# Optimization experiments

Hardware: AMD Instinct MI355X
Metric: run time of the kernel (lower is better)

Reference implementation:

```python
import jax, jax.numpy as jnp
import numpy as np

EPS = 1e-5

def conv(x, w, stride=1, pad=0, groups=1):
    # x: NCHW, w: OIHW
    return jax.lax.conv_general_dilated(
        x, w, window_strides=(stride, stride),
        padding=[(pad, pad), (pad, pad)],
        dimension_numbers=("NCHW", "OIHW", "NCHW"),
        feature_group_count=groups)

def bn_eval(x, gamma, beta, mean, var):
    scale = (gamma / jnp.sqrt(var + EPS))[None, :, None, None]
    shift = (beta - mean * gamma / jnp.sqrt(var + EPS))[None, :, None, None]
    return x * scale + shift

def setup_inputs() -> dict:
    key = jax.random.key(0)
    ks = jax.random.split(key, 12)
    B, Cin, H, W = 32, 64, 56, 56
    hidden, red, Cout, K = 384, 16, 64, 3
    f32 = jnp.float32
    x = jax.random.normal(ks[0], (B, Cin, H, W), dtype=f32)
    w_exp = jax.random.normal(ks[1], (hidden, Cin, 3, 3), dtype=f32) * 0.05
    w_dw  = jax.random.normal(ks[2], (hidden, 1, K, K), dtype=f32) * 0.1
    w_se1 = jax.random.normal(ks[3], (red, hidden, 1, 1), dtype=f32) * 0.05
    w_se2 = jax.random.normal(ks[4], (hidden, red, 1, 1), dtype=f32) * 0.1
    w_pw  = jax.random.normal(ks[5], (Cout, hidden, 1, 1), dtype=f32) * 0.05
    def bn_params(k, c):
        k1, k2 = jax.random.split(k)
        return (jnp.ones((c,), f32), jnp.zeros((c,), f32),
                jax.random.normal(k1, (c,), dtype=f32) * 0.01,
                jax.random.uniform(k2, (c,), dtype=f32, minval=0.5, maxval=1.5))
    g1, b1, m1, v1 = bn_params(ks[6], hidden)
    g2, b2, m2, v2 = bn_params(ks[7], hidden)
    g3, b3, m3, v3 = bn_params(ks[8], Cout)
    return dict(x=x, w_exp=w_exp, g1=g1, b1=b1, m1=m1, v1=v1,
                w_dw=w_dw, g2=g2, b2=b2, m2=m2, v2=v2,
                w_se1=w_se1, w_se2=w_se2, w_pw=w_pw,
                g3=g3, b3=b3, m3=m3, v3=v3)

def reference(x, w_exp, g1, b1, m1, v1, w_dw, g2, b2, m2, v2,
              w_se1, w_se2, w_pw, g3, b3, m3, v3):
    hidden = w_exp.shape[0]
    # expand conv (3x3) + BN + SiLU
    h = jax.nn.silu(bn_eval(conv(x, w_exp, stride=1, pad=1), g1, b1, m1, v1))
    # depthwise conv + BN + SiLU
    d = jax.nn.silu(bn_eval(conv(h, w_dw, stride=1, pad=1, groups=hidden), g2, b2, m2, v2))
    # squeeze-excitation: global avg pool -> 1x1 -> SiLU -> 1x1 -> sigmoid -> scale
    s = jnp.mean(d, axis=(2, 3), keepdims=True)            # [B, hidden, 1, 1]
    s = jax.nn.silu(conv(s, w_se1))
    s = jax.nn.sigmoid(conv(s, w_se2))
    d = d * s
    # pointwise projection + BN
    y = bn_eval(conv(d, w_pw), g3, b3, m3, v3)
    # eval mode: stochastic_depth is identity; quant_skip == (identity-quantized) input
    return y + x
```

## Files before the change

### kernel.cpp

```cpp
#include <hip/hip_runtime.h>

typedef unsigned short u16;
typedef unsigned int u32;
typedef __attribute__((ext_vector_type(2))) u32 u32x2;
typedef __attribute__((ext_vector_type(4))) u32 u32x4;
typedef __attribute__((ext_vector_type(2))) float f32x2;
typedef __attribute__((ext_vector_type(4))) float f32x4;
typedef __attribute__((ext_vector_type(8))) short s16x8;

#define DEV __device__ __forceinline__

DEV float bflo(u32 u){ union{u32 i; float f;} c; c.i = u << 16; return c.f; }
DEV float bfhi(u32 u){ union{u32 i; float f;} c; c.i = u & 0xffff0000u; return c.f; }
DEV u16 f2b(float f){
  union{float f; u32 u;} c; c.f = f;
  u32 u = c.u;
  u32 r = (u + 0x7fffu + ((u >> 16) & 1u)) >> 16;
  return (u16)r;
}
DEV float fsilu(float v){ return v / (1.f + __expf(-v)); }

typedef const __attribute__((address_space(1))) u32 gu32;
typedef __attribute__((address_space(3))) u32 lu32;
DEV void gload16(const u32* g, u32* l) {
  __builtin_amdgcn_global_load_lds((gu32*)g, (lu32*)l, 16, 0, 0);
}

constexpr int Bn = 32, Cin = 64, H = 56, Wd = 56, HID = 384, CO = 64;
constexpr int HW = H * Wd;
constexpr float EPS = 1e-5f;

constexpr int XROW = 72 * 64;
constexpr int WTAP = 128 * 64;
constexpr int WOCT = 9 * WTAP;
constexpr int XTROW = 72 * 64;

__global__ __launch_bounds__(256) void k_prep_wbn(
    const float* __restrict__ w,
    const float* __restrict__ g1, const float* __restrict__ b1,
    const float* __restrict__ m1, const float* __restrict__ v1,
    const float* __restrict__ g3, const float* __restrict__ b3,
    const float* __restrict__ m3, const float* __restrict__ v3,
    u16* __restrict__ wt,
    float* __restrict__ sc1, float* __restrict__ sh1,
    float* __restrict__ sc3, float* __restrict__ sh3)
{
  const int blk = blockIdx.x;
  if (blk < 864) {
    int t = blk * 256 + threadIdx.x;
    int octile = t / WOCT, r = t - octile * WOCT;
    int tap = r / WTAP, r2 = r - tap * WTAP;
    int ocl = r2 >> 6, col = r2 & 63;
    int physo = col >> 3, j = col & 7;
    int olog = physo ^ (ocl & 7);
    int ic = olog * 8 + j;
    int oc = octile * 128 + ocl;
    wt[t] = f2b(w[(oc * Cin + ic) * 9 + tap]);
  } else {
    for (int t = threadIdx.x; t < HID; t += 256) {
      float sc = g1[t] * rsqrtf(v1[t] + EPS);
      sc1[t] = sc;
      sh1[t] = b1[t] - m1[t] * sc;
    }
    if (threadIdx.x < CO) {
      int t = threadIdx.x;
      float sc = g3[t] * rsqrtf(v3[t] + EPS);
      sc3[t] = sc;
      sh3[t] = b3[t] - m3[t] * sc;
    }
  }
}

__global__ __launch_bounds__(256) void k_prep_x(
    const float* __restrict__ x, u16* __restrict__ xt, int b0)
{
  const int row = blockIdx.x;
  const int b = blockIdx.y, gb = b0 + b;
  const int tid = threadIdx.x;
  u16* dst = xt + ((size_t)b * 58 + row) * XTROW;
  if (row == 0 || row == 57) {
    for (int i = tid; i < 2304; i += 256) ((u32*)dst)[i] = 0;
    return;
  }
  const int y = row - 1;
  __shared__ u16 sx[64 * 58];
  {
    const int ic = tid >> 2, seg = tid & 3;
    const float* xp = x + ((size_t)(gb * Cin + ic) * H + y) * Wd + seg * 14;
    #pragma unroll
    for (int t = 0; t < 14; ++t) sx[ic * 58 + seg * 14 + t] = f2b(xp[t]);
  }
  __syncthreads();
  #pragma unroll
  for (int it = 0; it < 18; ++it) {
    const int slot = it * 4 + (tid >> 6);
    const int j = tid & 63;
    u16 v = 0;
    if (slot >= 1 && slot <= 56) {
      int ic = (((j >> 3) ^ (slot & 7)) << 3) | (j & 7);
      v = sx[ic * 58 + (slot - 1)];
    }
    dst[slot * 64 + j] = v;
  }
}

__global__ __launch_bounds__(256, 2) void k_expand_mfma(
    const u16* __restrict__ xt, const u16* __restrict__ wt,
    const float* __restrict__ sc1, const float* __restrict__ sh1,
    u16* __restrict__ h, int b0)
{
  (void)b0;
  __shared__ u16 sB[4 * XROW];
  __shared__ u16 sA[2][WTAP];
  const int tid = threadIdx.x;
  const int ypair = blockIdx.x, b = blockIdx.y;
  const int y0 = ypair * 2;
  const int wave = tid >> 6, ln = tid & 63;
  const int wm = wave >> 1, wn = wave & 1;
  const int lane15 = ln & 15, quad = ln >> 4;

  {
    const u32* xsrc = (const u32*)(xt + ((size_t)b * 58 + y0) * XTROW);
    #pragma unroll
    for (int it = 0; it < 9; ++it) {
      int chunk = it * 256 + tid;
      gload16(xsrc + chunk * 4, (u32*)sB + (chunk & ~63) * 4);
    }
    const u32* wsrc = (const u32*)wt;
    #pragma unroll
    for (int it = 0; it < 4; ++it) {
      int chunk = it * 256 + tid;
      gload16(wsrc + chunk * 4, (u32*)sA[0] + (chunk & ~63) * 4);
    }
  }
  __syncthreads();

  const int y = y0 + wn;

  for (int octile = 0; octile < 3; ++octile) {
    f32x4 acc[4][4];
    #pragma unroll
    for (int ms = 0; ms < 4; ++ms)
      #pragma unroll
      for (int ns = 0; ns < 4; ++ns) acc[ms][ns] = (f32x4){0.f, 0.f, 0.f, 0.f};

    #pragma unroll
    for (int tap = 0; tap < 9; ++tap) {
      const int step = octile * 9 + tap;
      const int buf = (octile + tap) & 1;

      u32x4 pf0, pf1, pf2, pf3;
      const bool pre = (step < 26);
      if (pre) {
        const u16* wnx = wt + (size_t)(step + 1) * WTAP;
        pf0 = *(const u32x4*)&wnx[(0 * 256 + tid) * 8];
        pf1 = *(const u32x4*)&wnx[(1 * 256 + tid) * 8];
        pf2 = *(const u32x4*)&wnx[(2 * 256 + tid) * 8];
        pf3 = *(const u32x4*)&wnx[(3 * 256 + tid) * 8];
      }

      constexpr int dyv[9] = {0,0,0,1,1,1,2,2,2};
      constexpr int dxv[9] = {0,1,2,0,1,2,0,1,2};
      const int dy = dyv[tap], dx = dxv[tap];
      const u16* sAc = sA[buf];
      __builtin_amdgcn_s_setprio(1);
      #pragma unroll
      for (int kk = 0; kk < 2; ++kk) {
        s16x8 af[4], bf[4];
        #pragma unroll
        for (int ms = 0; ms < 4; ++ms) {
          int ocl = wm * 64 + ms * 16 + lane15;
          int po = (kk * 4 + quad) ^ (ocl & 7);
          af[ms] = *(const s16x8*)&sAc[ocl * 64 + po * 8];
        }
        #pragma unroll
        for (int ns = 0; ns < 4; ++ns) {
          int row = wn + dy;
          int slot = ns * 16 + lane15 + dx;
          int po = (kk * 4 + quad) ^ (slot & 7);
          bf[ns] = *(const s16x8*)&sB[(row * 72 + slot) * 64 + po * 8];
        }
        #pragma unroll
        for (int ms = 0; ms < 4; ++ms)
          #pragma unroll
          for (int ns = 0; ns < 4; ++ns)
            acc[ms][ns] = __builtin_amdgcn_mfma_f32_16x16x32_bf16(
                af[ms], bf[ns], acc[ms][ns], 0, 0, 0);
      }
      __builtin_amdgcn_s_setprio(0);

      if (pre) {
        u16* sAn = sA[buf ^ 1];
        *(u32x4*)&sAn[(0 * 256 + tid) * 8] = pf0;
        *(u32x4*)&sAn[(1 * 256 + tid) * 8] = pf1;
        *(u32x4*)&sAn[(2 * 256 + tid) * 8] = pf2;
        *(u32x4*)&sAn[(3 * 256 + tid) * 8] = pf3;
      }
      __syncthreads();
    }

    #pragma unroll
    for (int ms = 0; ms < 4; ++ms) {
      int oc0 = octile * 128 + wm * 64 + ms * 16 + quad * 4;
      f32x4 sc = *(const f32x4*)&sc1[oc0];
      f32x4 sh = *(const f32x4*)&sh1[oc0];
      float scr[4] = {sc.x, sc.y, sc.z, sc.w};
      float shr[4] = {sh.x, sh.y, sh.z, sh.w};
      #pragma unroll
      for (int ns = 0; ns < 4; ++ns) {
        int xg = ns * 16 + lane15;
        if (xg < Wd) {
          float av[4] = {acc[ms][ns].x, acc[ms][ns].y, acc[ms][ns].z, acc[ms][ns].w};
          #pragma unroll
          for (int r = 0; r < 4; ++r) {
            float val = fsilu(av[r] * scr[r] + shr[r]);
            h[((size_t)(b * HID + oc0 + r) * H + y) * Wd + xg] = f2b(val);
          }
        }
      }
    }
  }
}

__global__ __launch_bounds__(256) void k_dw(
    const u16* __restrict__ h, const float* __restrict__ wdw,
    const float* __restrict__ g2, const float* __restrict__ b2,
    const float* __restrict__ m2, const float* __restrict__ v2,
    u16* __restrict__ d, float* __restrict__ mean)
{
  __shared__ float red[4];
  const int tid = threadIdx.x;
  const int c = blockIdx.x, b = blockIdx.y;
  const u32* hp32 = (const u32*)(h + (size_t)(b * HID + c) * HW);

  f32x2 wv2[9];
  #pragma unroll
  for (int t = 0; t < 9; ++t) {
    float w = wdw[c * 9 + t];
    wv2[t] = (f32x2){w, w};
  }
  const float sc = g2[c] * rsqrtf(v2[c] + EPS);
  const float sh = b2[c] - m2[c] * sc;
  const f32x2 scv = (f32x2){sc, sc}, shv = (f32x2){sh, sh};

  float lsum = 0.f;
  if (tid < 224) {
    const int r7 = tid / 28;
    const int wd = tid - r7 * 28;
    const int r0 = r7 * 7;
    u32* dp32 = (u32*)(d + (size_t)(b * HID + c) * HW);

    auto loadrow = [&](int rr, f32x2* P) {
      u32 m = 0, c0 = 0, p = 0;
      if (rr >= 0 && rr < 56) {
        const u32* rp = hp32 + rr * 28;
        c0 = rp[wd];
        if (wd > 0)  m = rp[wd - 1];
        if (wd < 27) p = rp[wd + 1];
      }
      float f_hm = bfhi(m), f_lc = bflo(c0), f_hc = bfhi(c0), f_lp = bflo(p);
      P[0] = (f32x2){f_hm, f_lc};
      P[1] = (f32x2){f_lc, f_hc};
      P[2] = (f32x2){f_hc, f_lp};
    };

    f32x2 Pa[3], Pb[3], Pc[3];
    loadrow(r0 - 1, Pa);
    loadrow(r0,     Pb);
    f32x2 ls2 = (f32x2){0.f, 0.f};
    #pragma unroll
    for (int i = 0; i < 7; ++i) {
      loadrow(r0 + i + 1, Pc);
      f32x2 s = (f32x2){0.f, 0.f};
      #pragma unroll
      for (int dx = 0; dx < 3; ++dx) s = __builtin_elementwise_fma(Pa[dx], wv2[dx], s);
      #pragma unroll
      for (int dx = 0; dx < 3; ++dx) s = __builtin_elementwise_fma(Pb[dx], wv2[3 + dx], s);
      #pragma unroll
      for (int dx = 0; dx < 3; ++dx) s = __builtin_elementwise_fma(Pc[dx], wv2[6 + dx], s);
      f32x2 t = __builtin_elementwise_fma(s, scv, shv);
      f32x2 val;
      val.x = fsilu(t.x);
      val.y = fsilu(t.y);
      ls2 += val;
      u32 pk;
      asm("v_cvt_pk_bf16_f32 %0, %1, %2" : "=v"(pk) : "v"(val.x), "v"(val.y));
      dp32[(r0 + i) * 28 + wd] = pk;
      #pragma unroll
      for (int q = 0; q < 3; ++q) { Pa[q] = Pb[q]; Pb[q] = Pc[q]; }
    }
    lsum = ls2.x + ls2.y;
  }

  #pragma unroll
  for (int off = 32; off > 0; off >>= 1) lsum += __shfl_down(lsum, off);
  if ((tid & 63) == 0) red[tid >> 6] = lsum;
  __syncthreads();
  if (tid == 0)
    mean[b * HID + c] = (red[0] + red[1] + red[2] + red[3]) * (1.f / 3136.f);
}

constexpr int PWP = 392;

__global__ __launch_bounds__(256, 2) void k_pw_mfma(
    const u16* __restrict__ d, const float* __restrict__ mean,
    const float* __restrict__ w1, const float* __restrict__ w2,
    const float* __restrict__ wpw,
    const float* __restrict__ sc3, const float* __restrict__ sh3,
    const float* __restrict__ x, float* __restrict__ out, int b0)
{
  __shared__ u16 sAw[64 * PWP];
  __shared__ u32 dtw[4 * 1024];
  __shared__ float smn[HID];
  __shared__ float sps[16 * 17];
  __shared__ float ss1[16];
  __shared__ float ssf[HID];
  const int tid = threadIdx.x;
  const int b = blockIdx.y, gb = b0 + b;
  const int p0 = blockIdx.x * 256;
  const int wave = tid >> 6, ln = tid & 63;
  const int lane15 = ln & 15, quad = ln >> 4;

  for (int c = tid; c < HID; c += 256) smn[c] = mean[b * HID + c];
  __syncthreads();
  {
    int r = tid >> 4, j = tid & 15;
    float p = 0.f;
    for (int c = j; c < HID; c += 16) p += smn[c] * w1[r * HID + c];
    sps[r * 17 + j] = p;
  }
  __syncthreads();
  if (tid < 16) {
    float s = 0.f;
    #pragma unroll
    for (int q = 0; q < 16; ++q) s += sps[tid * 17 + q];
    ss1[tid] = fsilu(s);
  }
  __syncthreads();
  for (int c = tid; c < HID; c += 256) {
    float s = 0.f;
    #pragma unroll
    for (int q = 0; q < 16; ++q) s += ss1[q] * w2[c * 16 + q];
    ssf[c] = 1.f / (1.f + __expf(-s));
  }
  __syncthreads();

  {
    for (int i = tid; i < 6144; i += 256) {
      int e = i * 4, co = e / 384, k = e - co * 384;
      f32x4 wv = *(const f32x4*)&wpw[e];
      f32x4 sf = *(const f32x4*)&ssf[k];
      float s3 = sc3[co];
      u32x2 pk;
      pk.x = (u32)f2b(wv.x * sf.x * s3) | ((u32)f2b(wv.y * sf.y * s3) << 16);
      pk.y = (u32)f2b(wv.z * sf.z * s3) | ((u32)f2b(wv.w * sf.w * s3) << 16);
      *(u32x2*)&sAw[co * PWP + k] = pk;
    }
  }
  __syncthreads();

  f32x4 acc[4][4];
  #pragma unroll
  for (int ms = 0; ms < 4; ++ms)
    #pragma unroll
    for (int ns = 0; ns < 4; ++ns) acc[ms][ns] = (f32x4){0.f, 0.f, 0.f, 0.f};

  const int cpair8 = ln >> 3;
  const int pxo = (ln & 7) * 8;
  const int swz = ln & 3;
  const int pbase = p0 + wave * 64;
  u32* mydt = &dtw[wave * 1024];
  const bool ld_ok = (pbase + pxo + 8 <= HW);
  const u16* dbase = d + (size_t)b * HID * HW + pbase + pxo;

  u32x4 pr0[2], pr1[2];
  #pragma unroll
  for (int ci = 0; ci < 2; ++ci) {
    pr0[ci] = (u32x4){0,0,0,0}; pr1[ci] = (u32x4){0,0,0,0};
    if (ld_ok) {
      int c = 2 * (ci * 8 + cpair8);
      const u16* dpp = dbase + (size_t)c * HW;
      pr0[ci] = *(const u32x4*)dpp;
      pr1[ci] = *(const u32x4*)(dpp + HW);
    }
  }

  for (int ks = 0; ks < 12; ++ks) {
    #pragma unroll
    for (int ci = 0; ci < 2; ++ci) {
      int k4 = ci * 2 + (cpair8 >> 2);
      u32* w0 = &mydt[pxo * 16 + ((k4 ^ swz) << 2) + (cpair8 & 3)];
      u32x4 r0 = pr0[ci], r1 = pr1[ci];
      w0[0 * 16] = (r0.x & 0xffffu) | (r1.x << 16);
      w0[1 * 16] = (r0.x >> 16)     | (r1.x & 0xffff0000u);
      w0[2 * 16] = (r0.y & 0xffffu) | (r1.y << 16);
      w0[3 * 16] = (r0.y >> 16)     | (r1.y & 0xffff0000u);
      w0[4 * 16] = (r0.z & 0xffffu) | (r1.z << 16);
      w0[5 * 16] = (r0.z >> 16)     | (r1.z & 0xffff0000u);
      w0[6 * 16] = (r0.w & 0xffffu) | (r1.w << 16);
      w0[7 * 16] = (r0.w >> 16)     | (r1.w & 0xffff0000u);
    }
    if (ks < 11) {
      #pragma unroll
      for (int ci = 0; ci < 2; ++ci) {
        if (ld_ok) {
          int c = (ks + 1) * 32 + 2 * (ci * 8 + cpair8);
          const u16* dpp = dbase + (size_t)c * HW;
          pr0[ci] = *(const u32x4*)dpp;
          pr1[ci] = *(const u32x4*)(dpp + HW);
        }
      }
    }
    const int k0 = ks * 32;
    s16x8 af[4], bf[4];
    #pragma unroll
    for (int ms = 0; ms < 4; ++ms) {
      int ocl = ms * 16 + lane15;
      af[ms] = *(const s16x8*)&sAw[ocl * PWP + k0 + quad * 8];
    }
    #pragma unroll
    for (int ns = 0; ns < 4; ++ns) {
      int pxl = ns * 16 + lane15;
      int p4 = quad ^ ((pxl >> 3) & 3);
      bf[ns] = *(const s16x8*)((const u16*)mydt + pxl * 32 + p4 * 8);
    }
    #pragma unroll
    for (int ms = 0; ms < 4; ++ms)
      #pragma unroll
      for (int ns = 0; ns < 4; ++ns)
        acc[ms][ns] = __builtin_amdgcn_mfma_f32_16x16x32_bf16(
            af[ms], bf[ns], acc[ms][ns], 0, 0, 0);
  }

  #pragma unroll
  for (int ns = 0; ns < 4; ++ns) {
    int p = pbase + ns * 16 + lane15;
    if (p < HW) {
      #pragma unroll
      for (int ms = 0; ms < 4; ++ms) {
        int co0 = ms * 16 + quad * 4;
        float av[4] = {acc[ms][ns].x, acc[ms][ns].y, acc[ms][ns].z, acc[ms][ns].w};
        #pragma unroll
        for (int r = 0; r < 4; ++r) {
          size_t idx = (size_t)(gb * CO + co0 + r) * HW + p;
          out[idx] = av[r] + sh3[co0 + r] + x[idx];
        }
      }
    }
  }
}

extern "C" void kernel_launch(void* const* d_in, const int* in_sizes, int n_in,
                              void* d_out, int out_size, void* d_ws, size_t ws_size,
                              hipStream_t stream)
{
  (void)in_sizes; (void)n_in; (void)out_size;
  const float* x     = (const float*)d_in[0];
  const float* w_exp = (const float*)d_in[1];
  const float* g1 = (const float*)d_in[2];
  const float* b1 = (const float*)d_in[3];
  const float* m1 = (const float*)d_in[4];
  const float* v1 = (const float*)d_in[5];
  const float* w_dw = (const float*)d_in[6];
  const float* g2 = (const float*)d_in[7];
  const float* b2 = (const float*)d_in[8];
  const float* m2 = (const float*)d_in[9];
  const float* v2 = (const float*)d_in[10];
  const float* w_se1 = (const float*)d_in[11];
  const float* w_se2 = (const float*)d_in[12];
  const float* w_pw  = (const float*)d_in[13];
  const float* g3 = (const float*)d_in[14];
  const float* b3 = (const float*)d_in[15];
  const float* m3 = (const float*)d_in[16];
  const float* v3 = (const float*)d_in[17];

  const size_t perB = (size_t)HID * HW * 2 * 2 + HID * 4 + (size_t)58 * XTROW * 2;
  const size_t fixed = 221184 * 2 + HID * 8 + CO * 8;
  int bc = Bn;
  while (bc > 1 && fixed + (size_t)bc * perB > ws_size) bc >>= 1;

  u16* wt = (u16*)d_ws;
  float* sc1 = (float*)(wt + 221184);
  float* sh1 = sc1 + HID;
  float* sc3 = sh1 + HID;
  float* sh3 = sc3 + CO;
  u16* h  = (u16*)(sh3 + CO);
  u16* dd = h + (size_t)bc * HID * HW;
  float* mean = (float*)(dd + (size_t)bc * HID * HW);
  u16* xt = (u16*)(mean + (size_t)bc * HID);

  k_prep_wbn<<<865, 256, 0, stream>>>(w_exp, g1, b1, m1, v1, g3, b3, m3, v3,
                                      wt, sc1, sh1, sc3, sh3);

  for (int b0 = 0; b0 < Bn; b0 += bc) {
    k_prep_x<<<dim3(58, bc), 256, 0, stream>>>(x, xt, b0);
    k_expand_mfma<<<dim3(28, bc), 256, 0, stream>>>(xt, wt, sc1, sh1, h, b0);
    k_dw<<<dim3(HID, bc), 256, 0, stream>>>(h, w_dw, g2, b2, m2, v2, dd, mean);
    k_pw_mfma<<<dim3(13, bc), 256, 0, stream>>>(dd, mean, w_se1, w_se2, w_pw,
                                                sc3, sh3, x, (float*)d_out, b0);
  }
}
```

Before: 263.5 us.

## Stage depthwise input in LDS and hoist SE weight folding into separate kernel

The depthwise kernel now copies each channel plane of h into shared memory with async global-to-LDS loads, so the stencil reads neighbouring columns from LDS instead of making repeated global loads. The squeeze-excitation MLP and the folding of the SE scale into the pointwise weights move out of k_pw_mfma, which previously repeated them in all 13 blocks per batch. A new per-batch kernel k_se_fold does this once and writes packed bf16 weights that the pointwise kernel loads with async copies. This costs one extra kernel launch per chunk and some extra workspace.

```diff
diff --git a/kernel.cpp b/kernel.cpp
--- a/kernel.cpp
+++ b/kernel.cpp
@@ -34,6 +34,7 @@
 constexpr int WTAP = 128 * 64;
 constexpr int WOCT = 9 * WTAP;
 constexpr int XTROW = 72 * 64;
+constexpr int PWP = 392;
 
 __global__ __launch_bounds__(256) void k_prep_wbn(
     const float* __restrict__ w,
@@ -228,10 +229,17 @@
     const float* __restrict__ m2, const float* __restrict__ v2,
     u16* __restrict__ d, float* __restrict__ mean)
 {
+  __shared__ u32 sdw[1568];
   __shared__ float red[4];
   const int tid = threadIdx.x;
   const int c = blockIdx.x, b = blockIdx.y;
   const u32* hp32 = (const u32*)(h + (size_t)(b * HID + c) * HW);
+
+  gload16(hp32 + tid * 4, sdw + (tid & ~63) * 4);
+  if (tid < 136) {
+    int chunk = 256 + tid;
+    gload16(hp32 + chunk * 4, sdw + (chunk & ~63) * 4);
+  }
 
   f32x2 wv2[9];
   #pragma unroll
@@ -242,6 +250,8 @@
   const float sc = g2[c] * rsqrtf(v2[c] + EPS);
   const float sh = b2[c] - m2[c] * sc;
   const f32x2 scv = (f32x2){sc, sc}, shv = (f32x2){sh, sh};
+
+  __syncthreads();
 
   float lsum = 0.f;
   if (tid < 224) {
@@ -253,7 +263,7 @@
     auto loadrow = [&](int rr, f32x2* P) {
       u32 m = 0, c0 = 0, p = 0;
       if (rr >= 0 && rr < 56) {
-        const u32* rp = hp32 + rr * 28;
+        const u32* rp = sdw + rr * 28;
         c0 = rp[wd];
         if (wd > 0)  m = rp[wd - 1];
         if (wd < 27) p = rp[wd + 1];
@@ -300,61 +310,72 @@
     mean[b * HID + c] = (red[0] + red[1] + red[2] + red[3]) * (1.f / 3136.f);
 }
 
-constexpr int PWP = 392;
-
-__global__ __launch_bounds__(256, 2) void k_pw_mfma(
-    const u16* __restrict__ d, const float* __restrict__ mean,
-    const float* __restrict__ w1, const float* __restrict__ w2,
-    const float* __restrict__ wpw,
-    const float* __restrict__ sc3, const float* __restrict__ sh3,
-    const float* __restrict__ x, float* __restrict__ out, int b0)
-{
-  __shared__ u16 sAw[64 * PWP];
-  __shared__ u32 dtw[4 * 1024];
+__global__ __launch_bounds__(256) void k_se_fold(
+    const float* __restrict__ mean, const float* __restrict__ w1,
+    const float* __restrict__ w2, const float* __restrict__ wpw,
+    const float* __restrict__ sc3, u16* __restrict__ apk)
+{
   __shared__ float smn[HID];
   __shared__ float sps[16 * 17];
   __shared__ float ss1[16];
   __shared__ float ssf[HID];
+  const int b = blockIdx.x, tid = threadIdx.x;
+  for (int c = tid; c < HID; c += 256) smn[c] = mean[b * HID + c];
+  __syncthreads();
+  {
+    int r = tid >> 4, j = tid & 15;
+    float p = 0.f;
+    for (int c = j; c < HID; c += 16) p += smn[c] * w1[r * HID + c];
+    sps[r * 17 + j] = p;
+  }
+  __syncthreads();
+  if (tid < 16) {
+    float s = 0.f;
+    #pragma unroll
+    for (int q = 0; q < 16; ++q) s += sps[tid * 17 + q];
+    ss1[tid] = fsilu(s);
+  }
+  __syncthreads();
+  for (int c = tid; c < HID; c += 256) {
+    float s = 0.f;
+    #pragma unroll
+    for (int q = 0; q < 16; ++q) s += ss1[q] * w2[c * 16 + q];
+    ssf[c] = 1.f / (1.f + __expf(-s));
+  }
+  __syncthreads();
+  u16* ap = apk + (size_t)b * CO * PWP;
+  for (int i = tid; i < 6144; i += 256) {
+    int e = i * 4, co = e / 384, k = e - co * 384;
+    f32x4 wv = *(const f32x4*)&wpw[e];
+    f32x4 sf = *(const f32x4*)&ssf[k];
+    float s3 = sc3[co];
+    u32x2 pk;
+    pk.x = (u32)f2b(wv.x * sf.x * s3) | ((u32)f2b(wv.y * sf.y * s3) << 16);
+    pk.y = (u32)f2b(wv.z * sf.z * s3) | ((u32)f2b(wv.w * sf.w * s3) << 16);
+    *(u32x2*)&ap[co * PWP + k] = pk;
+  }
+}
+
+__global__ __launch_bounds__(256, 2) void k_pw_mfma(
+    const u16* __restrict__ d, const u16* __restrict__ apk,
+    const float* __restrict__ sh3,
+    const float* __restrict__ x, float* __restrict__ out, int b0)
+{
+  __shared__ u16 sAw[64 * PWP];
+  __shared__ u32 dtw[4 * 1024];
   const int tid = threadIdx.x;
   const int b = blockIdx.y, gb = b0 + b;
   const int p0 = blockIdx.x * 256;
   const int wave = tid >> 6, ln = tid & 63;
   const int lane15 = ln & 15, quad = ln >> 4;
 
-  for (int c = tid; c < HID; c += 256) smn[c] = mean[b * HID + c];
-  __syncthreads();
   {
-    int r = tid >> 4, j = tid & 15;
-    float p = 0.f;
-    for (int c = j; c < HID; c += 16) p += smn[c] * w1[r * HID + c];
-    sps[r * 17 + j] = p;
-  }
-  __syncthreads();
-  if (tid < 16) {
-    float s = 0.f;
-    #pragma unroll
-    for (int q = 0; q < 16; ++q) s += sps[tid * 17 + q];
-    ss1[tid] = fsilu(s);
-  }
-  __syncthreads();
-  for (int c = tid; c < HID; c += 256) {
-    float s = 0.f;
-    #pragma unroll
-    for (int q = 0; q < 16; ++q) s += ss1[q] * w2[c * 16 + q];
-    ssf[c] = 1.f / (1.f + __expf(-s));
-  }
-  __syncthreads();
-
-  {
-    for (int i = tid; i < 6144; i += 256) {
-      int e = i * 4, co = e / 384, k = e - co * 384;
-      f32x4 wv = *(const f32x4*)&wpw[e];
-      f32x4 sf = *(const f32x4*)&ssf[k];
-      float s3 = sc3[co];
-      u32x2 pk;
-      pk.x = (u32)f2b(wv.x * sf.x * s3) | ((u32)f2b(wv.y * sf.y * s3) << 16);
-      pk.y = (u32)f2b(wv.z * sf.z * s3) | ((u32)f2b(wv.w * sf.w * s3) << 16);
-      *(u32x2*)&sAw[co * PWP + k] = pk;
+    const u32* ap = (const u32*)(apk + (size_t)b * CO * PWP);
+    #pragma unroll
+    for (int i = 0; i < 13; ++i) {
+      int chunk = i * 256 + tid;
+      if (chunk < 3136)
+        gload16(ap + chunk * 4, (u32*)sAw + (chunk & ~63) * 4);
     }
   }
   __syncthreads();
@@ -474,7 +495,8 @@
   const float* m3 = (const float*)d_in[16];
   const float* v3 = (const float*)d_in[17];
 
-  const size_t perB = (size_t)HID * HW * 2 * 2 + HID * 4 + (size_t)58 * XTROW * 2;
+  const size_t perB = (size_t)HID * HW * 2 * 2 + HID * 4
+                    + (size_t)58 * XTROW * 2 + (size_t)CO * PWP * 2;
   const size_t fixed = 221184 * 2 + HID * 8 + CO * 8;
   int bc = Bn;
   while (bc > 1 && fixed + (size_t)bc * perB > ws_size) bc >>= 1;
@@ -488,6 +510,7 @@
   u16* dd = h + (size_t)bc * HID * HW;
   float* mean = (float*)(dd + (size_t)bc * HID * HW);
   u16* xt = (u16*)(mean + (size_t)bc * HID);
+  u16* apk = xt + (size_t)bc * 58 * XTROW;
 
   k_prep_wbn<<<865, 256, 0, stream>>>(w_exp, g1, b1, m1, v1, g3, b3, m3, v3,
                                       wt, sc1, sh1, sc3, sh3);
@@ -496,7 +519,8 @@
     k_prep_x<<<dim3(58, bc), 256, 0, stream>>>(x, xt, b0);
     k_expand_mfma<<<dim3(28, bc), 256, 0, stream>>>(xt, wt, sc1, sh1, h, b0);
     k_dw<<<dim3(HID, bc), 256, 0, stream>>>(h, w_dw, g2, b2, m2, v2, dd, mean);
-    k_pw_mfma<<<dim3(13, bc), 256, 0, stream>>>(dd, mean, w_se1, w_se2, w_pw,
-                                                sc3, sh3, x, (float*)d_out, b0);
-  }
-}
+    k_se_fold<<<bc, 256, 0, stream>>>(mean, w_se1, w_se2, w_pw, sc3, apk);
+    k_pw_mfma<<<dim3(13, bc), 256, 0, stream>>>(dd, apk, sh3,
+                                                x, (float*)d_out, b0);
+  }
+}
```

Result: faster. 255.2 us (-3.1%).
